# Kernel tuning notes

Measured on AMD Instinct MI355X. Metric: run time of the kernel, lower is better.

The kernel has to match this reference:

```python
import jax, jax.numpy as jnp
import numpy as np


def setup_inputs() -> dict:
    key = jax.random.key(0)
    k1, k2 = jax.random.split(key)
    # x: [B, C_in, H, W]
    x = jax.random.normal(k1, (32, 256, 56, 56), dtype=jnp.float32)
    # weight: [C_out, C_in, kH, kW]; weight_init_std ~ small-std gaussian init
    weight = jax.random.normal(k2, (512, 256, 3, 3), dtype=jnp.float32) * 0.02
    return {"x": x, "weight": weight}


def reference(x, weight):
    # HebbianConv2d default inference path: out_sim = kernel_mult2d (plain conv2d,
    # stride 1, VALID padding), out_act = identity, out_bias=False, out_cmp=False,
    # weight_zeta_mode=None so get_weight() == weight.
    y = jax.lax.conv_general_dilated(
        x, weight,
        window_strides=(1, 1),
        padding="VALID",
        dimension_numbers=("NCHW", "OIHW", "NCHW"),
    )  # [B, C_out, H-kH+1, W-kW+1] = [32, 512, 54, 54]
    return y
```

## Files before the change

### kernel.cpp

```cpp
#include <hip/hip_runtime.h>

typedef __attribute__((ext_vector_type(8))) short short8;
typedef __attribute__((ext_vector_type(4))) float f32x4;

#define B_    32
#define CI_   256
#define H_    56
#define HW_   3136
#define CO_   512
#define OHW_  54
#define PIXB_ 2916
#define NPIX_ 93312

#define XT_BYTES 51380224ull
#define WS_NEED  53739520ull

__device__ __forceinline__ ushort f2bf(float f) {
  unsigned u = __float_as_uint(f);
  unsigned r = (u + 0x7FFFu + ((u >> 16) & 1u)) >> 16;
  return (ushort)r;
}

__device__ __forceinline__ void async16(const void* g, void* l) {
  __builtin_amdgcn_global_load_lds(
      (const __attribute__((address_space(1))) unsigned int*)g,
      (__attribute__((address_space(3))) unsigned int*)l, 16, 0, 0);
}

#define CIP 260
__global__ __launch_bounds__(256)
void transpose_x(const float* __restrict__ x, ushort* __restrict__ xt) {
  __shared__ ushort tile[64 * CIP];
  const int b = blockIdx.y, hw0 = blockIdx.x * 64;
  const int t = threadIdx.x;
  const int j = t & 15, q = t >> 4;
  const int hw4 = j * 4;
  const float* xb = x + (size_t)b * CI_ * HW_ + hw0;

  #pragma unroll
  for (int p = 0; p < 4; ++p) {
    const int c0 = p * 64 + q * 4;
    float4 v[4];
    #pragma unroll
    for (int r = 0; r < 4; ++r)
      v[r] = *(const float4*)(xb + (size_t)(c0 + r) * HW_ + hw4);
    #pragma unroll
    for (int r2 = 0; r2 < 4; ++r2) {
      ushort4 o;
      o.x = f2bf(((const float*)&v[0])[r2]);
      o.y = f2bf(((const float*)&v[1])[r2]);
      o.z = f2bf(((const float*)&v[2])[r2]);
      o.w = f2bf(((const float*)&v[3])[r2]);
      *(ushort4*)&tile[(hw4 + r2) * CIP + c0] = o;
    }
  }
  __syncthreads();

  ushort* ob = xt + ((size_t)b * HW_ + hw0) * CI_;
  #pragma unroll
  for (int p = 0; p < 8; ++p) {
    const int hw  = p * 8 + (t >> 5);
    const int ci8 = (t & 31) * 8;
    const ushort* src = &tile[hw * CIP + ci8];
    uint2 lo = *(const uint2*)src;
    uint2 hi = *(const uint2*)(src + 4);
    uint4 v; v.x = lo.x; v.y = lo.y; v.z = hi.x; v.w = hi.y;
    *(uint4*)(ob + (size_t)hw * CI_ + ci8) = v;
  }
}

__global__ __launch_bounds__(256)
void repack_w(const float* __restrict__ w, ushort* __restrict__ wt) {
  __shared__ float buf[2304];
  const int co = blockIdx.x, t = threadIdx.x;
  const float* wp = w + (size_t)co * 2304;
  #pragma unroll
  for (int p = 0; p < 9; ++p) buf[p * 256 + t] = wp[p * 256 + t];
  __syncthreads();
  #pragma unroll
  for (int k = 0; k < 9; ++k)
    wt[(size_t)k * CO_ * CI_ + (size_t)co * CI_ + t] = f2bf(buf[t * 9 + k]);
}

__global__ __launch_bounds__(256, 3)
void conv_mfma(const ushort* __restrict__ xt, const ushort* __restrict__ wt,
               float* __restrict__ out) {
  __shared__ ushort lds_w[128 * 32];
  __shared__ ushort lds_x[128 * 32];

  const int t    = threadIdx.x;
  const int lane = t & 63;
  const int wv   = t >> 6;
  const int quad = lane >> 4;
  const int l16  = lane & 15;
  const int co0  = (blockIdx.x & 3) * 128;
  const int P0   = (blockIdx.x >> 2) * 128;

  const int row0 = wv * 32 + (lane >> 2);
  const int ci8  = (lane & 3) * 8;

  const size_t wA0 = (size_t)(co0 + row0) * CI_ + ci8;
  const size_t wA1 = (size_t)(co0 + row0 + 16) * CI_ + ci8;

  int P_a = P0 + row0;
  int b_a = P_a / PIXB_; int rem_a = P_a - b_a * PIXB_;
  int oh_a = rem_a / OHW_; int ow_a = rem_a - oh_a * OHW_;
  const size_t xB0 = ((size_t)b_a * HW_ + oh_a * H_ + ow_a) * CI_ + ci8;
  int P_b = P_a + 16;
  int b_b = P_b / PIXB_; int rem_b = P_b - b_b * PIXB_;
  int oh_b = rem_b / OHW_; int ow_b = rem_b - oh_b * OHW_;
  const size_t xB1 = ((size_t)b_b * HW_ + oh_b * H_ + ow_b) * CI_ + ci8;

  char* ldsw_c = (char*)lds_w + wv * 2048;
  char* ldsx_c = (char*)lds_x + wv * 2048;

  f32x4 acc[4][4];
  #pragma unroll
  for (int i = 0; i < 4; ++i)
    #pragma unroll
    for (int j = 0; j < 4; ++j) acc[i][j] = (f32x4){0.f, 0.f, 0.f, 0.f};

  const int wm = (wv & 1) * 64;
  const int wn = (wv >> 1) * 64;

  for (int khkw = 0; khkw < 9; ++khkw) {
    const int kh = khkw / 3, kw = khkw - kh * 3;
    const size_t w_off = (size_t)khkw * CO_ * CI_;
    const size_t x_off = (size_t)(kh * H_ + kw) * CI_;
    for (int ci0 = 0; ci0 < CI_; ci0 += 32) {
      async16(wt + wA0 + w_off + ci0, ldsw_c);
      async16(wt + wA1 + w_off + ci0, ldsw_c + 1024);
      async16(xt + xB0 + x_off + ci0, ldsx_c);
      async16(xt + xB1 + x_off + ci0, ldsx_c + 1024);
      __syncthreads();

      short8 af[4], bfr[4];
      #pragma unroll
      for (int mt = 0; mt < 4; ++mt)
        af[mt] = *(const short8*)&lds_w[(wm + mt * 16 + l16) * 32 + quad * 8];
      #pragma unroll
      for (int nt = 0; nt < 4; ++nt)
        bfr[nt] = *(const short8*)&lds_x[(wn + nt * 16 + l16) * 32 + quad * 8];
      #pragma unroll
      for (int mt = 0; mt < 4; ++mt)
        #pragma unroll
        for (int nt = 0; nt < 4; ++nt)
          acc[mt][nt] = __builtin_amdgcn_mfma_f32_16x16x32_bf16(
              af[mt], bfr[nt], acc[mt][nt], 0, 0, 0);

      __syncthreads();
    }
  }

  #pragma unroll
  for (int nt = 0; nt < 4; ++nt) {
    int P = P0 + wn + nt * 16 + l16;
    int b = P / PIXB_; int rem = P - b * PIXB_;
    size_t obase = (size_t)b * (CO_ * PIXB_) + rem;
    #pragma unroll
    for (int mt = 0; mt < 4; ++mt) {
      int cobase = co0 + wm + mt * 16 + quad * 4;
      #pragma unroll
      for (int r = 0; r < 4; ++r)
        out[obase + (size_t)(cobase + r) * PIXB_] = acc[mt][nt][r];
    }
  }
}

__global__ void naive_conv(const float* __restrict__ x, const float* __restrict__ w,
                           float* __restrict__ out) {
  size_t i = (size_t)blockIdx.x * 256 + threadIdx.x;
  if (i >= (size_t)47775744ull) return;
  int ow = (int)(i % OHW_); size_t r = i / OHW_;
  int oh = (int)(r % OHW_); r /= OHW_;
  int co = (int)(r % CO_);  int b = (int)(r / CO_);
  const float* xp = x + (size_t)b * CI_ * HW_;
  const float* wp = w + (size_t)co * CI_ * 9;
  float acc = 0.f;
  for (int ci = 0; ci < CI_; ++ci) {
    const float* xr = xp + (size_t)ci * HW_ + oh * H_ + ow;
    const float* wr = wp + ci * 9;
    #pragma unroll
    for (int kh = 0; kh < 3; ++kh)
      #pragma unroll
      for (int kw = 0; kw < 3; ++kw)
        acc += xr[kh * H_ + kw] * wr[kh * 3 + kw];
  }
  out[i] = acc;
}

extern "C" void kernel_launch(void* const* d_in, const int* in_sizes, int n_in,
                              void* d_out, int out_size, void* d_ws, size_t ws_size,
                              hipStream_t stream) {
  const float* x = (const float*)d_in[0];
  const float* w = (const float*)d_in[1];
  float* out = (float*)d_out;

  if (ws_size >= WS_NEED) {
    ushort* xt = (ushort*)d_ws;
    ushort* wt = (ushort*)((char*)d_ws + XT_BYTES);
    transpose_x<<<dim3(49, 32), 256, 0, stream>>>(x, xt);
    repack_w<<<dim3(512), 256, 0, stream>>>(w, wt);
    conv_mfma<<<dim3(2916), 256, 0, stream>>>(xt, wt, out);
  } else {
    naive_conv<<<(47775744 + 255) / 256, 256, 0, stream>>>(x, w, out);
  }
}
```

Before: 556.8 us.

## Triple-buffer async LDS pipeline with larger 256x128 tiles and XCD remap

Rewrites the conv GEMM main loop to use 512-thread blocks with a 256x128 output tile and a K step of 64. Global-to-LDS async loads are triple-buffered and prefetched two steps ahead, which replaces the old per-step load-then-syncthreads pattern. LDS rows are XOR-swizzled to avoid bank conflicts, and block indices are remapped per XCD for cache locality. MFMA sections also raise wave priority with setprio. The cost is 144KB of LDS per block and hand-placed barriers and waitcnt counts that must stay exactly right.

```diff
diff --git a/kernel.cpp b/kernel.cpp
--- a/kernel.cpp
+++ b/kernel.cpp
@@ -82,37 +82,52 @@
     wt[(size_t)k * CO_ * CI_ + (size_t)co * CI_ + t] = f2bf(buf[t * 9 + k]);
 }
 
-__global__ __launch_bounds__(256, 3)
+#define NT_    36
+#define BUFSZ_ 49152
+#define BOFF_  32768
+#define NBLK_  1458
+
+__global__ __launch_bounds__(512, 2)
 void conv_mfma(const ushort* __restrict__ xt, const ushort* __restrict__ wt,
                float* __restrict__ out) {
-  __shared__ ushort lds_w[128 * 32];
-  __shared__ ushort lds_x[128 * 32];
-
-  const int t    = threadIdx.x;
-  const int lane = t & 63;
-  const int wv   = t >> 6;
-  const int quad = lane >> 4;
-  const int l16  = lane & 15;
-  const int co0  = (blockIdx.x & 3) * 128;
-  const int P0   = (blockIdx.x >> 2) * 128;
-
-  const int row0 = wv * 32 + (lane >> 2);
-  const int ci8  = (lane & 3) * 8;
-
-  const size_t wA0 = (size_t)(co0 + row0) * CI_ + ci8;
-  const size_t wA1 = (size_t)(co0 + row0 + 16) * CI_ + ci8;
-
-  int P_a = P0 + row0;
-  int b_a = P_a / PIXB_; int rem_a = P_a - b_a * PIXB_;
-  int oh_a = rem_a / OHW_; int ow_a = rem_a - oh_a * OHW_;
-  const size_t xB0 = ((size_t)b_a * HW_ + oh_a * H_ + ow_a) * CI_ + ci8;
-  int P_b = P_a + 16;
-  int b_b = P_b / PIXB_; int rem_b = P_b - b_b * PIXB_;
-  int oh_b = rem_b / OHW_; int ow_b = rem_b - oh_b * OHW_;
-  const size_t xB1 = ((size_t)b_b * HW_ + oh_b * H_ + ow_b) * CI_ + ci8;
-
-  char* ldsw_c = (char*)lds_w + wv * 2048;
-  char* ldsx_c = (char*)lds_x + wv * 2048;
+  __shared__ __align__(128) char lds[3 * BUFSZ_];
+
+  const int tid  = threadIdx.x;
+  const int l    = tid & 63;
+  const int wv   = tid >> 6;
+  const int quad = l >> 4;
+  const int l16  = l & 15;
+  const int lr   = l >> 3;
+  const int lc   = l & 7;
+  const int cswz = (lc ^ lr) << 3;
+
+  const int q8 = 182, r8 = 2;
+  const int xcd = blockIdx.x & 7;
+  const int idx = blockIdx.x >> 3;
+  const int logical =
+      (xcd < r8 ? xcd * (q8 + 1) : r8 * (q8 + 1) + (xcd - r8) * q8) + idx;
+  const int co0 = (logical & 1) << 8;
+  const int P0  = (logical >> 1) << 7;
+
+  const size_t wbaseA = (size_t)(co0 + wv * 8 + lr) * CI_ + cswz;
+  size_t xbase[2];
+  #pragma unroll
+  for (int r = 0; r < 2; ++r) {
+    int P = P0 + r * 64 + wv * 8 + lr;
+    int b = P / PIXB_; int rem = P - b * PIXB_;
+    int oh = rem / OHW_; int ow = rem - oh * OHW_;
+    xbase[r] = ((size_t)b * HW_ + oh * H_ + ow) * CI_ + cswz;
+  }
+
+  const int wm  = (wv & 3) << 6;
+  const int wn  = (wv >> 2) << 6;
+  const int sA0 = (quad << 4) ^ ((l16 & 7) << 4);
+  int raoff[4], rboff[4];
+  #pragma unroll
+  for (int i = 0; i < 4; ++i) {
+    raoff[i] = (wm + i * 16 + l16) * 128 + sA0;
+    rboff[i] = BOFF_ + (wn + i * 16 + l16) * 128 + sA0;
+  }
 
   f32x4 acc[4][4];
   #pragma unroll
@@ -120,36 +135,73 @@
     #pragma unroll
     for (int j = 0; j < 4; ++j) acc[i][j] = (f32x4){0.f, 0.f, 0.f, 0.f};
 
-  const int wm = (wv & 1) * 64;
-  const int wn = (wv >> 1) * 64;
-
-  for (int khkw = 0; khkw < 9; ++khkw) {
-    const int kh = khkw / 3, kw = khkw - kh * 3;
-    const size_t w_off = (size_t)khkw * CO_ * CI_;
-    const size_t x_off = (size_t)(kh * H_ + kw) * CI_;
-    for (int ci0 = 0; ci0 < CI_; ci0 += 32) {
-      async16(wt + wA0 + w_off + ci0, ldsw_c);
-      async16(wt + wA1 + w_off + ci0, ldsw_c + 1024);
-      async16(xt + xB0 + x_off + ci0, ldsx_c);
-      async16(xt + xB1 + x_off + ci0, ldsx_c + 1024);
-      __syncthreads();
-
-      short8 af[4], bfr[4];
-      #pragma unroll
-      for (int mt = 0; mt < 4; ++mt)
-        af[mt] = *(const short8*)&lds_w[(wm + mt * 16 + l16) * 32 + quad * 8];
+  auto issueA2 = [&](int buf, int tt, int r0) {
+    const int k2 = tt >> 2; const int c2 = (tt & 3) << 6;
+    const ushort* src = wt + (size_t)k2 * (CO_ * CI_) + wbaseA + c2;
+    char* dst = lds + buf * BUFSZ_ + wv * 1024;
+    async16(src + (size_t)(r0 << 6) * CI_,       dst + r0 * 8192);
+    async16(src + (size_t)((r0 + 1) << 6) * CI_, dst + (r0 + 1) * 8192);
+  };
+  auto issueB1 = [&](int buf, int tt, int r) {
+    const int k2 = tt >> 2; const int c2 = (tt & 3) << 6;
+    const int kh2 = k2 / 3, kw2 = k2 - kh2 * 3;
+    async16(xt + xbase[r] + (size_t)(kh2 * H_ + kw2) * CI_ + c2,
+            lds + buf * BUFSZ_ + BOFF_ + r * 8192 + wv * 1024);
+  };
+
+  issueA2(0, 0, 0); issueA2(0, 0, 2); issueB1(0, 0, 0); issueB1(0, 0, 1);
+  issueA2(1, 1, 0); issueA2(1, 1, 2); issueB1(1, 1, 0); issueB1(1, 1, 1);
+
+  int cur = 0;
+  for (int t = 0; t < NT_; ++t) {
+    if (t == NT_ - 1) asm volatile("s_waitcnt vmcnt(0)" ::: "memory");
+    else              asm volatile("s_waitcnt vmcnt(6)" ::: "memory");
+    __builtin_amdgcn_sched_barrier(0);
+    __builtin_amdgcn_s_barrier();
+    asm volatile("" ::: "memory");
+
+    const char* ab  = lds + cur * BUFSZ_;
+    const int ibuf  = (cur == 0) ? 2 : cur - 1;
+    const bool pf   = (t < NT_ - 2);
+
+    short8 af[4], bfr[4];
+    #pragma unroll
+    for (int i = 0; i < 4; ++i) {
+      af[i]  = *(const short8*)(ab + raoff[i]);
+      bfr[i] = *(const short8*)(ab + rboff[i]);
+    }
+    if (pf) { issueA2(ibuf, t + 2, 0); issueB1(ibuf, t + 2, 0); }
+    asm volatile("" ::: "memory");
+    __builtin_amdgcn_s_barrier();
+    asm volatile("" ::: "memory");
+    __builtin_amdgcn_s_setprio(1);
+    #pragma unroll
+    for (int mt = 0; mt < 4; ++mt)
       #pragma unroll
       for (int nt = 0; nt < 4; ++nt)
-        bfr[nt] = *(const short8*)&lds_x[(wn + nt * 16 + l16) * 32 + quad * 8];
-      #pragma unroll
-      for (int mt = 0; mt < 4; ++mt)
-        #pragma unroll
-        for (int nt = 0; nt < 4; ++nt)
-          acc[mt][nt] = __builtin_amdgcn_mfma_f32_16x16x32_bf16(
-              af[mt], bfr[nt], acc[mt][nt], 0, 0, 0);
-
-      __syncthreads();
-    }
+        acc[mt][nt] = __builtin_amdgcn_mfma_f32_16x16x32_bf16(
+            af[mt], bfr[nt], acc[mt][nt], 0, 0, 0);
+    __builtin_amdgcn_s_setprio(0);
+
+    #pragma unroll
+    for (int i = 0; i < 4; ++i) {
+      af[i]  = *(const short8*)(ab + (raoff[i] ^ 64));
+      bfr[i] = *(const short8*)(ab + (rboff[i] ^ 64));
+    }
+    if (pf) { issueA2(ibuf, t + 2, 2); issueB1(ibuf, t + 2, 1); }
+    asm volatile("" ::: "memory");
+    __builtin_amdgcn_s_barrier();
+    asm volatile("" ::: "memory");
+    __builtin_amdgcn_s_setprio(1);
+    #pragma unroll
+    for (int mt = 0; mt < 4; ++mt)
+      #pragma unroll
+      for (int nt = 0; nt < 4; ++nt)
+        acc[mt][nt] = __builtin_amdgcn_mfma_f32_16x16x32_bf16(
+            af[mt], bfr[nt], acc[mt][nt], 0, 0, 0);
+    __builtin_amdgcn_s_setprio(0);
+
+    cur = (cur == 2) ? 0 : cur + 1;
   }
 
   #pragma unroll
@@ -201,7 +253,7 @@
     ushort* wt = (ushort*)((char*)d_ws + XT_BYTES);
     transpose_x<<<dim3(49, 32), 256, 0, stream>>>(x, xt);
     repack_w<<<dim3(512), 256, 0, stream>>>(w, wt);
-    conv_mfma<<<dim3(2916), 256, 0, stream>>>(xt, wt, out);
+    conv_mfma<<<dim3(NBLK_), 512, 0, stream>>>(xt, wt, out);
   } else {
     naive_conv<<<(47775744 + 255) / 256, 256, 0, stream>>>(x, w, out);
   }
```

After: 498.6 us. 10.4% less time.
